# Performance work log

Measured on AMD Instinct MI355X. Metric: run time of the kernel, lower is better.

The kernel has to match this reference:

```python
import jax, jax.numpy as jnp
import numpy as np

B, DIM = 64, 131072


def setup_inputs() -> dict:
    key = jax.random.key(0)
    k1, k2, k3 = jax.random.split(key, 3)
    z = jax.random.normal(k1, (B, DIM), dtype=jnp.float32)
    trace_in = jax.random.normal(k2, (B, DIM), dtype=jnp.float32)
    ctrl = jax.random.normal(k3, (B, 3), dtype=jnp.float32)
    return {"z": z, "trace_in": trace_in, "ctrl": ctrl}


def reference(z, trace_in, ctrl):
    # gates: [B,1]
    store = jax.nn.sigmoid(ctrl[:, 0:1])
    retrieve = jax.nn.sigmoid(ctrl[:, 1:2])
    # clear gate only touches the internal buffer (no effect on outputs); omitted.

    # global max-abs normalization (single scalar, as in torch: z.abs().max())
    z_norm = z / (jnp.abs(z).max() + 1e-6)

    z_f = jnp.fft.fft(z_norm)          # [B,DIM] complex64
    trace_f = jnp.fft.fft(trace_in)    # [B,DIM] complex64
    new_trace_f = trace_f + z_f * store
    new_trace = jnp.fft.ifft(new_trace_f)
    read = jnp.fft.ifft(new_trace_f * jnp.conj(z_f)) * retrieve

    dummy_ptr = jnp.zeros((z.shape[0], 1), dtype=jnp.float32)
    return (read, new_trace, dummy_ptr, jnp.array(1.0, dtype=jnp.float32))
```

## Files before the change

### kernel.cpp

```cpp
#include <hip/hip_runtime.h>
#include <math.h>

#define NROW 64
#define DIM  131072

struct cf { float x, y; };
__device__ __forceinline__ cf cadd(cf a, cf b){ return {a.x+b.x, a.y+b.y}; }
__device__ __forceinline__ cf csub(cf a, cf b){ return {a.x-b.x, a.y-b.y}; }
__device__ __forceinline__ cf cmul(cf a, cf b){ return {a.x*b.x - a.y*b.y, a.x*b.y + a.y*b.x}; }
template<int SG> __device__ __forceinline__ cf muli(cf a){
  return (SG > 0) ? cf{-a.y, a.x} : cf{a.y, -a.x};
}
__device__ __forceinline__ float sigmoidf(float x){ return 1.0f/(1.0f + __expf(-x)); }

__device__ __forceinline__ void wsync(){
  __builtin_amdgcn_wave_barrier();
  asm volatile("" ::: "memory");
}

typedef float __attribute__((ext_vector_type(4))) fvec4;

template<int SG> __device__ __forceinline__ void fft4(cf&a0, cf&a1, cf&a2, cf&a3){
  cf e0=cadd(a0,a2), e1=csub(a0,a2), o0=cadd(a1,a3), o1=csub(a1,a3);
  cf w=muli<SG>(o1);
  a0=cadd(e0,o0); a2=csub(e0,o0); a1=cadd(e1,w); a3=csub(e1,w);
}

template<int SG> __device__ __forceinline__ void fft8(cf v[8]){
  cf e0=v[0], e1=v[2], e2=v[4], e3=v[6];
  cf o0=v[1], o1=v[3], o2=v[5], o3=v[7];
  fft4<SG>(e0,e1,e2,e3); fft4<SG>(o0,o1,o2,o3);
  const float R=0.70710678118654752f;
  cf w1=cmul(o1, cf{R, (float)SG*R});
  cf w2=muli<SG>(o2);
  cf w3=cmul(o3, cf{-R, (float)SG*R});
  v[0]=cadd(e0,o0); v[4]=csub(e0,o0);
  v[1]=cadd(e1,w1); v[5]=csub(e1,w1);
  v[2]=cadd(e2,w2); v[6]=csub(e2,w2);
  v[3]=cadd(e3,w3); v[7]=csub(e3,w3);
}

template<int SG> __device__ __forceinline__ void fft16(cf v[16]){
  cf e[8], o[8];
  #pragma unroll
  for(int i=0;i<8;i++){ e[i]=v[2*i]; o[i]=v[2*i+1]; }
  fft8<SG>(e); fft8<SG>(o);
  const float C[8]={1.f,0.92387953251128674f,0.70710678118654752f,0.38268343236508977f,
                    0.f,-0.38268343236508977f,-0.70710678118654752f,-0.92387953251128674f};
  const float S[8]={0.f,0.38268343236508977f,0.70710678118654752f,0.92387953251128674f,
                    1.f,0.92387953251128674f,0.70710678118654752f,0.38268343236508977f};
  #pragma unroll
  for(int k=0;k<8;k++){
    cf w=cmul(o[k], cf{C[k], (float)SG*S[k]});
    v[k]=cadd(e[k],w); v[k+8]=csub(e[k],w);
  }
}

__global__ void k0_tail(float* __restrict__ dout, int cplx){
  int t = threadIdx.x;
  size_t base = (size_t)2*NROW*DIM*cplx;
  if(t < NROW) dout[base + t] = 0.f;
  else if(t == NROW) dout[base + NROW] = 1.0f;
}

__global__ __launch_bounds__(256) void k1_maxabs(const float* __restrict__ z, unsigned* __restrict__ dst){
  __shared__ float red[256];
  size_t i0 = (size_t)blockIdx.x*blockDim.x + threadIdx.x;
  size_t stride = (size_t)gridDim.x*blockDim.x;
  const float4* z4 = (const float4*)z;
  size_t n4 = (size_t)NROW*DIM/4;
  float m = 0.f;
  for(size_t i=i0;i<n4;i+=stride){
    float4 v=z4[i];
    m = fmaxf(m, fmaxf(fmaxf(fabsf(v.x),fabsf(v.y)), fmaxf(fabsf(v.z),fabsf(v.w))));
  }
  red[threadIdx.x]=m; __syncthreads();
  #pragma unroll
  for(int s=128;s>0;s>>=1){
    if(threadIdx.x<(unsigned)s) red[threadIdx.x]=fmaxf(red[threadIdx.x],red[threadIdx.x+s]);
    __syncthreads();
  }
  if(threadIdx.x==0) atomicMax(dst, __float_as_uint(red[0]));
}

__global__ __launch_bounds__(256) void k2_fwd1(
    const float* __restrict__ z, const float* __restrict__ tr,
    const float* __restrict__ ctrl, const unsigned* __restrict__ maxbits,
    float2* __restrict__ Bws, float* __restrict__ out_nt, int cplx)
{
  __shared__ float reb[4384], imb[4384];
  __shared__ float twc[256], tws[256];
  int t = threadIdx.x;
  int b = blockIdx.x >> 5;
  int n1b = (blockIdx.x & 31) << 4;
  {
    float sv, cv;
    __sincosf(-0.0245436926061703f * (float)t, &sv, &cv);
    twc[t]=cv; tws[t]=sv;
  }
  float s = 1.0f/(__uint_as_float(*maxbits) + 1e-6f);
  float gs = sigmoidf(ctrl[b*3+0]);
  float cc = gs*s;
  const float4* zr4 = (const float4*)(z  + (size_t)b*DIM);
  const float4* tr4 = (const float4*)(tr + (size_t)b*DIM);
  #pragma unroll
  for(int it=0; it<4; ++it){
    int e = t + 256*it;
    int n2 = e >> 2, j4 = e & 3;
    int fi = n2*128 + (n1b>>2) + j4;
    float4 zv = zr4[fi];
    float4 tv = tr4[fi];
    int lb = n2*17 + j4*4;
    reb[lb+0]=zv.x; reb[lb+1]=zv.y; reb[lb+2]=zv.z; reb[lb+3]=zv.w;
    imb[lb+0]=tv.x; imb[lb+1]=tv.y; imb[lb+2]=tv.z; imb[lb+3]=tv.w;
    float n0 = fmaf(cc, zv.x, tv.x);
    float n1v= fmaf(cc, zv.y, tv.y);
    float n2v= fmaf(cc, zv.z, tv.z);
    float n3 = fmaf(cc, zv.w, tv.w);
    size_t n = (size_t)n2*512 + n1b + j4*4;
    size_t oidx = (size_t)b*DIM + n;
    if(cplx == 2){
      fvec4 a  = {n0, 0.f, n1v, 0.f};
      fvec4 bq = {n2v, 0.f, n3, 0.f};
      fvec4* op = (fvec4*)((float2*)out_nt + oidx);
      __builtin_nontemporal_store(a,  op);
      __builtin_nontemporal_store(bq, op+1);
    } else {
      out_nt[oidx+0]=n0; out_nt[oidx+1]=n1v; out_nt[oidx+2]=n2v; out_nt[oidx+3]=n3;
    }
  }
  __syncthreads();
  int f = t & 15, p = t >> 4;
  cf v[16];
  #pragma unroll
  for(int q=0;q<16;q++){ int n2=q*16+p; v[q].x=reb[n2*17+f]; v[q].y=imb[n2*17+f]; }
  fft16<-1>(v);
  #pragma unroll
  for(int kq=1;kq<16;kq++){ int tt=(p*kq)&255; v[kq]=cmul(v[kq], cf{twc[tt], tws[tt]}); }
  __syncthreads();
  #pragma unroll
  for(int kq=0;kq<16;kq++){ reb[f*274 + kq*17 + p]=v[kq].x; imb[f*274 + kq*17 + p]=v[kq].y; }
  __syncthreads();
  #pragma unroll
  for(int pp=0;pp<16;pp++){ v[pp].x=reb[f*274 + p*17 + pp]; v[pp].y=imb[f*274 + p*17 + pp]; }
  fft16<-1>(v);
  int nn1 = n1b + f;
  cf w, st;
  {
    float sv, cv;
    __sincosf(-4.793689960382698e-05f * (float)(nn1*p), &sv, &cv);
    w = {cv, sv};
    __sincosf(-4.793689960382698e-05f * 16.f * (float)nn1, &sv, &cv);
    st = {cv, sv};
  }
  #pragma unroll
  for(int kp=0;kp<16;kp++){
    int k2 = kp*16 + p;
    cf r = cmul(v[kp], w);
    Bws[((size_t)b<<17) + (size_t)k2*512 + nn1] = make_float2(r.x, r.y);
    w = cmul(w, st);
  }
}

template<int SG>
__device__ __forceinline__ void fft512_wave(
    float* Cre, float* Cim, int lane, const float* twc, const float* tws)
{
  cf v[8];
  int kQ = lane>>3, pp = lane&7;
  #pragma unroll
  for(int q=0;q<8;q++){ v[q].x=Cre[q*64+lane]; v[q].y=Cim[q*64+lane]; }
  fft8<SG>(v);
  #pragma unroll
  for(int kq=1;kq<8;kq++){
    int tt=(lane*kq)&511; int ti=tt&255; float sg=(tt&256)?-1.f:1.f;
    v[kq]=cmul(v[kq], cf{sg*twc[ti], (float)SG*sg*tws[ti]});
  }
  wsync();
  #pragma unroll
  for(int kq=0;kq<8;kq++){ Cre[lane*9+kq]=v[kq].x; Cim[lane*9+kq]=v[kq].y; }
  wsync();
  #pragma unroll
  for(int q=0;q<8;q++){ int idx=(q*8+pp)*9+kQ; v[q].x=Cre[idx]; v[q].y=Cim[idx]; }
  fft8<SG>(v);
  #pragma unroll
  for(int kq=1;kq<8;kq++){
    int tt=(pp*kq*8)&511; int ti=tt&255; float sg=(tt&256)?-1.f:1.f;
    v[kq]=cmul(v[kq], cf{sg*twc[ti], (float)SG*sg*tws[ti]});
  }
  wsync();
  #pragma unroll
  for(int kq=0;kq<8;kq++){ Cre[pp*73+kq*9+kQ]=v[kq].x; Cim[pp*73+kq*9+kQ]=v[kq].y; }
  wsync();
  #pragma unroll
  for(int p2=0;p2<8;p2++){ int idx=p2*73 + kQ*9 + pp; v[p2].x=Cre[idx]; v[p2].y=Cim[idx]; }
  fft8<SG>(v);
  wsync();
  #pragma unroll
  for(int kp=0;kp<8;kp++){ int k=kp*64 + kQ*8 + pp; Cre[k]=v[kp].x; Cim[k]=v[kp].y; }
  wsync();
}

__global__ __launch_bounds__(128) void k3_mid(
    float2* __restrict__ Bws, const float* __restrict__ ctrl,
    const unsigned* __restrict__ maxbits)
{
  __shared__ float Cbuf[2][1168];
  __shared__ float twc[256], tws[256];
  int t = threadIdx.x;
  int bp = blockIdx.x >> 7;
  int pr = blockIdx.x & 127;
  int b0 = bp*2, b1 = b0+1;
  int cA = (pr==0) ? 0   : pr;
  int cB = (pr==0) ? 128 : 256-pr;
  int col = t >> 6, lane = t & 63;
  int myc = col ? cB : cA;
  for(int i=t;i<256;i+=128){
    float sv,cv; __sincosf(0.0122718463030851f*(float)i, &sv, &cv);
    twc[i]=cv; tws[i]=sv;
  }
  float s = 1.0f/(__uint_as_float(*maxbits)+1e-6f);
  float gs0 = sigmoidf(ctrl[b0*3+0]);
  float al0 = sigmoidf(ctrl[b0*3+1]) * (1.0f/(float)DIM);
  float gs1 = sigmoidf(ctrl[b1*3+0]);
  float al1 = sigmoidf(ctrl[b1*3+1]) * (1.0f/(float)DIM);
  float* Cre = Cbuf[col]; float* Cim = Cre + 584;
  const float* Pre = (pr==0) ? Cre : Cbuf[1-col];
  const float* Pim = Pre + 584;
  float2* colp0 = Bws + ((size_t)b0<<17) + ((size_t)myc<<9);
  float2* colp1 = Bws + ((size_t)b1<<17) + ((size_t)myc<<9);
  cf pv0[8], pv1[8];

  {
    const float4* c4 = (const float4*)colp0;
    #pragma unroll
    for(int r=0;r<4;r++){
      float4 q = c4[lane + 64*r];
      int j = 2*(lane + 64*r);
      Cre[j]=q.x;   Cim[j]=q.y;
      Cre[j+1]=q.z; Cim[j+1]=q.w;
    }
  }
  __syncthreads();
  fft512_wave<-1>(Cre, Cim, lane, twc, tws);
  __syncthreads();
  #pragma unroll
  for(int rr=0;rr<8;rr++){
    int k1  = lane + 64*rr;
    int k1p = (myc==0) ? ((512-k1)&511) : (511-k1);
    float cr = Cre[k1], ci = Cim[k1];
    float qr = Pre[k1p], qi = -Pim[k1p];
    float zur = 0.5f*(cr+qr), zui = 0.5f*(ci+qi);
    float dr = cr-qr, di = ci-qi;
    float tfr = 0.5f*di, tfi = -0.5f*dr;
    float szr = s*zur, szi = s*zui;
    float ntr = fmaf(gs0, szr, tfr), nti = fmaf(gs0, szi, tfi);
    pv0[rr].x = (ntr*szr + nti*szi)*al0;
    pv0[rr].y = (nti*szr - ntr*szi)*al0;
  }
  __syncthreads();

  {
    const float4* c4 = (const float4*)colp1;
    #pragma unroll
    for(int r=0;r<4;r++){
      float4 q = c4[lane + 64*r];
      int j = 2*(lane + 64*r);
      Cre[j]=q.x;   Cim[j]=q.y;
      Cre[j+1]=q.z; Cim[j+1]=q.w;
    }
  }
  wsync();
  fft512_wave<-1>(Cre, Cim, lane, twc, tws);
  __syncthreads();
  #pragma unroll
  for(int rr=0;rr<8;rr++){
    int k1  = lane + 64*rr;
    int k1p = (myc==0) ? ((512-k1)&511) : (511-k1);
    float cr = Cre[k1], ci = Cim[k1];
    float qr = Pre[k1p], qi = -Pim[k1p];
    float zur = 0.5f*(cr+qr), zui = 0.5f*(ci+qi);
    float dr = cr-qr, di = ci-qi;
    float tfr = 0.5f*di, tfi = -0.5f*dr;
    float szr = s*zur, szi = s*zui;
    float ntr = fmaf(gs1, szr, tfr), nti = fmaf(gs1, szi, tfi);
    pv1[rr].x = (ntr*szr + nti*szi)*al1;
    pv1[rr].y = (nti*szr - ntr*szi)*al1;
  }
  __syncthreads();

  #pragma unroll
  for(int rr=0;rr<8;rr++){
    int k1 = lane + 64*rr;
    Cre[k1] = pv0[rr].x - pv1[rr].y;
    Cim[k1] = pv0[rr].y + pv1[rr].x;
  }
  wsync();
  fft512_wave<1>(Cre, Cim, lane, twc, tws);
  cf w, st;
  {
    float sv,cv;
    __sincosf(4.793689960382698e-05f * (float)(lane*myc), &sv, &cv);
    w = {cv, sv};
    __sincosf(4.793689960382698e-05f * 64.f * (float)myc, &sv, &cv);
    st = {cv, sv};
  }
  #pragma unroll
  for(int rr=0;rr<8;rr++){
    int m1 = lane + 64*rr;
    cf r2 = cmul(cf{Cre[m1],Cim[m1]}, w);
    colp0[m1] = make_float2(r2.x, r2.y);
    w = cmul(w, st);
  }
}

__global__ __launch_bounds__(256) void k4_inv2(
    const float2* __restrict__ Qws, float* __restrict__ dout, int cplx)
{
  __shared__ float reb[4384], imb[4384];
  __shared__ float twc[256], tws[256];
  int t = threadIdx.x;
  int bp = blockIdx.x >> 5;
  int m1b = (blockIdx.x & 31) << 4;
  int b0 = bp*2;
  {
    float sv, cv;
    __sincosf(0.0245436926061703f * (float)t, &sv, &cv);
    twc[t]=cv; tws[t]=sv;
  }
  const float4* Qp = (const float4*)(Qws + ((size_t)b0<<17));
  #pragma unroll
  for(int it=0; it<8; ++it){
    int e = t + 256*it;
    int k2 = e >> 3, j = e & 7;
    float4 q = Qp[k2*256 + (m1b>>1) + j];
    int lb = k2*17 + 2*j;
    reb[lb+0]=q.x; imb[lb+0]=q.y;
    reb[lb+1]=q.z; imb[lb+1]=q.w;
  }
  __syncthreads();
  int f = t & 15, p = t >> 4;
  cf v[16];
  #pragma unroll
  for(int q=0;q<16;q++){ int k2=q*16+p; v[q].x=reb[k2*17+f]; v[q].y=imb[k2*17+f]; }
  fft16<1>(v);
  #pragma unroll
  for(int kq=1;kq<16;kq++){ int tt=(p*kq)&255; v[kq]=cmul(v[kq], cf{twc[tt], tws[tt]}); }
  __syncthreads();
  #pragma unroll
  for(int kq=0;kq<16;kq++){ reb[f*274+kq*17+p]=v[kq].x; imb[f*274+kq*17+p]=v[kq].y; }
  __syncthreads();
  #pragma unroll
  for(int pp=0;pp<16;pp++){ v[pp].x=reb[f*274+p*17+pp]; v[pp].y=imb[f*274+p*17+pp]; }
  fft16<1>(v);
  #pragma unroll
  for(int kp=0;kp<16;kp++){
    int m2 = kp*16 + p;
    size_t n = (size_t)(m1b + f) + (size_t)512*m2;
    size_t o0 = (size_t)b0*DIM + n;
    if(cplx==2){
      ((float2*)dout)[o0]       = make_float2(v[kp].x, 0.f);
      ((float2*)dout)[o0 + DIM] = make_float2(v[kp].y, 0.f);
    } else {
      dout[o0]       = v[kp].x;
      dout[o0 + DIM] = v[kp].y;
    }
  }
}

extern "C" void kernel_launch(void* const* d_in, const int* in_sizes, int n_in,
                              void* d_out, int out_size, void* d_ws, size_t ws_size,
                              hipStream_t stream)
{
  (void)in_sizes; (void)n_in; (void)ws_size;
  const float* z    = (const float*)d_in[0];
  const float* tr   = (const float*)d_in[1];
  const float* ctrl = (const float*)d_in[2];
  float* dout = (float*)d_out;
  int cplx = (out_size > 20000000) ? 2 : 1;
  unsigned* maxbits = (unsigned*)d_ws;
  float2* Bws = (float2*)((char*)d_ws + 256);

  hipMemsetAsync(d_ws, 0, 4, stream);
  hipLaunchKernelGGL(k0_tail,  dim3(1),    dim3(128), 0, stream, dout, cplx);
  hipLaunchKernelGGL(k1_maxabs,dim3(1024), dim3(256), 0, stream, z, maxbits);
  hipLaunchKernelGGL(k2_fwd1,  dim3(2048), dim3(256), 0, stream,
                     z, tr, ctrl, maxbits, Bws, dout + (size_t)NROW*DIM*cplx, cplx);
  hipLaunchKernelGGL(k3_mid,   dim3(4096), dim3(128), 0, stream, Bws, ctrl, maxbits);
  hipLaunchKernelGGL(k4_inv2,  dim3(1024), dim3(256), 0, stream, Bws, dout, cplx);
}
```

Measured before the change: 203.5 us.

## Fuse all stages into one cooperative persistent kernel with grid syncs

Replaces the memset plus five separate launches (tail, max-abs, forward FFT pass, middle FFT pass, inverse pass) with a single cooperative persistent kernel. Stages are separated by grid-wide syncs, and blocks loop over tiles. The global max is now a two-level reduction through per-block partials instead of an atomicMax. This removes launch gaps and per-kernel ramp-up, but adds grid barrier cost and fixes the grid size to the occupancy limit, which may lower per-stage parallelism or register headroom under the 4-blocks-per-CU launch bound.

```diff
diff --git a/kernel.cpp b/kernel.cpp
--- a/kernel.cpp
+++ b/kernel.cpp
@@ -1,5 +1,8 @@
 #include <hip/hip_runtime.h>
+#include <hip/hip_cooperative_groups.h>
 #include <math.h>
+
+namespace cg = cooperative_groups;
 
 #define NROW 64
 #define DIM  131072
@@ -56,49 +59,23 @@
   }
 }
 
-__global__ void k0_tail(float* __restrict__ dout, int cplx){
+
+__device__ __forceinline__ void k2_body(
+    float* __restrict__ S, int tile,
+    const float* __restrict__ z, const float* __restrict__ tr,
+    const float* __restrict__ ctrl, float s,
+    float2* __restrict__ Bws, float* __restrict__ out_nt, int cplx)
+{
+  float* reb = S; float* imb = S+4384; float* twc = S+8768; float* tws = S+9024;
   int t = threadIdx.x;
-  size_t base = (size_t)2*NROW*DIM*cplx;
-  if(t < NROW) dout[base + t] = 0.f;
-  else if(t == NROW) dout[base + NROW] = 1.0f;
-}
-
-__global__ __launch_bounds__(256) void k1_maxabs(const float* __restrict__ z, unsigned* __restrict__ dst){
-  __shared__ float red[256];
-  size_t i0 = (size_t)blockIdx.x*blockDim.x + threadIdx.x;
-  size_t stride = (size_t)gridDim.x*blockDim.x;
-  const float4* z4 = (const float4*)z;
-  size_t n4 = (size_t)NROW*DIM/4;
-  float m = 0.f;
-  for(size_t i=i0;i<n4;i+=stride){
-    float4 v=z4[i];
-    m = fmaxf(m, fmaxf(fmaxf(fabsf(v.x),fabsf(v.y)), fmaxf(fabsf(v.z),fabsf(v.w))));
-  }
-  red[threadIdx.x]=m; __syncthreads();
-  #pragma unroll
-  for(int s=128;s>0;s>>=1){
-    if(threadIdx.x<(unsigned)s) red[threadIdx.x]=fmaxf(red[threadIdx.x],red[threadIdx.x+s]);
-    __syncthreads();
-  }
-  if(threadIdx.x==0) atomicMax(dst, __float_as_uint(red[0]));
-}
-
-__global__ __launch_bounds__(256) void k2_fwd1(
-    const float* __restrict__ z, const float* __restrict__ tr,
-    const float* __restrict__ ctrl, const unsigned* __restrict__ maxbits,
-    float2* __restrict__ Bws, float* __restrict__ out_nt, int cplx)
-{
-  __shared__ float reb[4384], imb[4384];
-  __shared__ float twc[256], tws[256];
-  int t = threadIdx.x;
-  int b = blockIdx.x >> 5;
-  int n1b = (blockIdx.x & 31) << 4;
+  int b = tile >> 5;
+  int n1b = (tile & 31) << 4;
+  __syncthreads();
   {
     float sv, cv;
     __sincosf(-0.0245436926061703f * (float)t, &sv, &cv);
     twc[t]=cv; tws[t]=sv;
   }
-  float s = 1.0f/(__uint_as_float(*maxbits) + 1e-6f);
   float gs = sigmoidf(ctrl[b*3+0]);
   float cc = gs*s;
   const float4* zr4 = (const float4*)(z  + (size_t)b*DIM);
@@ -201,31 +178,23 @@
   wsync();
 }
 
-__global__ __launch_bounds__(128) void k3_mid(
-    float2* __restrict__ Bws, const float* __restrict__ ctrl,
-    const unsigned* __restrict__ maxbits)
-{
-  __shared__ float Cbuf[2][1168];
-  __shared__ float twc[256], tws[256];
-  int t = threadIdx.x;
-  int bp = blockIdx.x >> 7;
-  int pr = blockIdx.x & 127;
+__device__ __forceinline__ void k3_tile(
+    float* __restrict__ Cb, const float* __restrict__ twc, const float* __restrict__ tws,
+    int tile, int col, int lane, float s,
+    float2* __restrict__ Bws, const float* __restrict__ ctrl)
+{
+  int bp = tile >> 7;
+  int pr = tile & 127;
   int b0 = bp*2, b1 = b0+1;
   int cA = (pr==0) ? 0   : pr;
   int cB = (pr==0) ? 128 : 256-pr;
-  int col = t >> 6, lane = t & 63;
   int myc = col ? cB : cA;
-  for(int i=t;i<256;i+=128){
-    float sv,cv; __sincosf(0.0122718463030851f*(float)i, &sv, &cv);
-    twc[i]=cv; tws[i]=sv;
-  }
-  float s = 1.0f/(__uint_as_float(*maxbits)+1e-6f);
   float gs0 = sigmoidf(ctrl[b0*3+0]);
   float al0 = sigmoidf(ctrl[b0*3+1]) * (1.0f/(float)DIM);
   float gs1 = sigmoidf(ctrl[b1*3+0]);
   float al1 = sigmoidf(ctrl[b1*3+1]) * (1.0f/(float)DIM);
-  float* Cre = Cbuf[col]; float* Cim = Cre + 584;
-  const float* Pre = (pr==0) ? Cre : Cbuf[1-col];
+  float* Cre = Cb + col*1168; float* Cim = Cre + 584;
+  const float* Pre = (pr==0) ? Cre : (Cb + (1-col)*1168);
   const float* Pim = Pre + 584;
   float2* colp0 = Bws + ((size_t)b0<<17) + ((size_t)myc<<9);
   float2* colp1 = Bws + ((size_t)b1<<17) + ((size_t)myc<<9);
@@ -314,15 +283,16 @@
   }
 }
 
-__global__ __launch_bounds__(256) void k4_inv2(
+__device__ __forceinline__ void k4_body(
+    float* __restrict__ S, int r,
     const float2* __restrict__ Qws, float* __restrict__ dout, int cplx)
 {
-  __shared__ float reb[4384], imb[4384];
-  __shared__ float twc[256], tws[256];
+  float* reb = S; float* imb = S+4384; float* twc = S+8768; float* tws = S+9024;
   int t = threadIdx.x;
-  int bp = blockIdx.x >> 5;
-  int m1b = (blockIdx.x & 31) << 4;
+  int bp = r >> 5;
+  int m1b = (r & 31) << 4;
   int b0 = bp*2;
+  __syncthreads();
   {
     float sv, cv;
     __sincosf(0.0245436926061703f * (float)t, &sv, &cv);
@@ -368,6 +338,75 @@
   }
 }
 
+__global__ __launch_bounds__(256, 4) void mega(
+    const float* __restrict__ z, const float* __restrict__ tr,
+    const float* __restrict__ ctrl, float* __restrict__ wsmax,
+    float2* __restrict__ Bws, float* __restrict__ out_nt,
+    float* __restrict__ dout, int cplx)
+{
+  __shared__ float S[9280];
+  cg::grid_group g = cg::this_grid();
+  int t = threadIdx.x, bid = blockIdx.x, nb = gridDim.x;
+
+  {
+    const float4* z4 = (const float4*)z;
+    size_t n4 = (size_t)NROW*DIM/4;
+    float m = 0.f;
+    for(size_t i=(size_t)bid*256+t; i<n4; i+=(size_t)nb*256){
+      float4 v=z4[i];
+      m = fmaxf(m, fmaxf(fmaxf(fabsf(v.x),fabsf(v.y)), fmaxf(fabsf(v.z),fabsf(v.w))));
+    }
+    S[t]=m; __syncthreads();
+    #pragma unroll
+    for(int st=128;st>0;st>>=1){
+      if(t<st) S[t]=fmaxf(S[t],S[t+st]);
+      __syncthreads();
+    }
+    if(t==0) wsmax[bid]=S[0];
+    if(bid==0){
+      size_t base = (size_t)2*NROW*DIM*cplx;
+      if(t < NROW) dout[base + t] = 0.f;
+      else if(t == NROW) dout[base + NROW] = 1.0f;
+    }
+  }
+  g.sync();
+
+  float s;
+  {
+    float m = 0.f;
+    for(int i=t;i<nb;i+=256) m = fmaxf(m, wsmax[i]);
+    S[t]=m; __syncthreads();
+    #pragma unroll
+    for(int st=128;st>0;st>>=1){
+      if(t<st) S[t]=fmaxf(S[t],S[t+st]);
+      __syncthreads();
+    }
+    s = 1.0f/(S[0] + 1e-6f);
+  }
+
+  for(int tile=bid; tile<2048; tile+=nb)
+    k2_body(S, tile, z, tr, ctrl, s, Bws, out_nt, cplx);
+  g.sync();
+
+  {
+    int h = t>>7, tt = t&127, col = tt>>6, lane = tt&63;
+    float* Cb  = S + h*2336;
+    float* twc3 = S + 4672; float* tws3 = S + 4928;
+    __syncthreads();
+    { float sv,cv; __sincosf(0.0122718463030851f*(float)t, &sv, &cv);
+      if(t<256){ twc3[t]=cv; tws3[t]=sv; } }
+    __syncthreads();
+    for(int p=bid; p<2048; p+=nb){
+      __syncthreads();
+      k3_tile(Cb, twc3, tws3, p*2+h, col, lane, s, Bws, ctrl);
+    }
+  }
+  g.sync();
+
+  for(int r=bid; r<1024; r+=nb)
+    k4_body(S, r, Bws, dout, cplx);
+}
+
 extern "C" void kernel_launch(void* const* d_in, const int* in_sizes, int n_in,
                               void* d_out, int out_size, void* d_ws, size_t ws_size,
                               hipStream_t stream)
@@ -378,14 +417,18 @@
   const float* ctrl = (const float*)d_in[2];
   float* dout = (float*)d_out;
   int cplx = (out_size > 20000000) ? 2 : 1;
-  unsigned* maxbits = (unsigned*)d_ws;
-  float2* Bws = (float2*)((char*)d_ws + 256);
-
-  hipMemsetAsync(d_ws, 0, 4, stream);
-  hipLaunchKernelGGL(k0_tail,  dim3(1),    dim3(128), 0, stream, dout, cplx);
-  hipLaunchKernelGGL(k1_maxabs,dim3(1024), dim3(256), 0, stream, z, maxbits);
-  hipLaunchKernelGGL(k2_fwd1,  dim3(2048), dim3(256), 0, stream,
-                     z, tr, ctrl, maxbits, Bws, dout + (size_t)NROW*DIM*cplx, cplx);
-  hipLaunchKernelGGL(k3_mid,   dim3(4096), dim3(128), 0, stream, Bws, ctrl, maxbits);
-  hipLaunchKernelGGL(k4_inv2,  dim3(1024), dim3(256), 0, stream, Bws, dout, cplx);
-}
+  float* wsmax = (float*)d_ws;
+  float2* Bws  = (float2*)((char*)d_ws + 8192);
+  float* out_nt = dout + (size_t)NROW*DIM*cplx;
+
+  int maxb = 0;
+  hipOccupancyMaxActiveBlocksPerMultiprocessor(&maxb, mega, 256, 0);
+  if(maxb < 1) maxb = 1;
+  if(maxb > 4) maxb = 4;
+  int grid = 256 * maxb;
+
+  void* args[] = { (void*)&z, (void*)&tr, (void*)&ctrl, (void*)&wsmax,
+                   (void*)&Bws, (void*)&out_nt, (void*)&dout, (void*)&cplx };
+  hipLaunchCooperativeKernel((const void*)mega, dim3(grid), dim3(256),
+                             args, 0, stream);
+}
```

Result: slower. 410.8 us (+101.8%).
